# Kernel optimization log

Measured on AMD Instinct MI355X. Metric: run time of the kernel, lower is better.

Reference implementation:

```python
import jax, jax.numpy as jnp
import numpy as np

DIM = 256
HEADS = 8
DIM_HEAD = 64
SLICE_NUM = 64
INNER = HEADS * DIM_HEAD
B, N = 4, 32768


def setup_inputs() -> dict:
    key = jax.random.key(0)
    ks = jax.random.split(key, 12)
    s_in = 1.0 / np.sqrt(DIM)
    s_h = 1.0 / np.sqrt(DIM_HEAD)
    s_o = 1.0 / np.sqrt(INNER)
    return {
        "x": jax.random.normal(ks[0], (B, N, DIM), dtype=jnp.float32),
        "Wfx": jax.random.normal(ks[1], (INNER, DIM), dtype=jnp.float32) * s_in,
        "bfx": jax.random.normal(ks[2], (INNER,), dtype=jnp.float32) * 0.01,
        "Wx": jax.random.normal(ks[3], (INNER, DIM), dtype=jnp.float32) * s_in,
        "bx": jax.random.normal(ks[4], (INNER,), dtype=jnp.float32) * 0.01,
        "Wslice": jax.random.normal(ks[5], (SLICE_NUM, DIM_HEAD), dtype=jnp.float32) * s_h,
        "bslice": jax.random.normal(ks[6], (SLICE_NUM,), dtype=jnp.float32) * 0.01,
        "temperature": jnp.ones((1, HEADS, 1, 1), dtype=jnp.float32) * 0.5,
        "Wq": jax.random.normal(ks[7], (DIM_HEAD, DIM_HEAD), dtype=jnp.float32) * s_h,
        "Wk": jax.random.normal(ks[8], (DIM_HEAD, DIM_HEAD), dtype=jnp.float32) * s_h,
        "Wv": jax.random.normal(ks[9], (DIM_HEAD, DIM_HEAD), dtype=jnp.float32) * s_h,
        "Wout": jax.random.normal(ks[10], (DIM, INNER), dtype=jnp.float32) * s_o,
        "bout": jax.random.normal(ks[11], (DIM,), dtype=jnp.float32) * 0.01,
    }


def reference(x, Wfx, bfx, Wx, bx, Wslice, bslice, temperature, Wq, Wk, Wv, Wout, bout):
    b, n, c = x.shape
    Ch = Wq.shape[0]
    H = Wfx.shape[0] // Ch
    # project and split heads: [B, H, N, Ch]
    fx_mid = (x @ Wfx.T + bfx).reshape(b, n, H, Ch).transpose(0, 2, 1, 3)
    x_mid = (x @ Wx.T + bx).reshape(b, n, H, Ch).transpose(0, 2, 1, 3)
    # soft slice assignment: [B, H, N, M]
    temp = jnp.clip(temperature, 0.1, 5.0)
    logits = (x_mid @ Wslice.T + bslice) / temp
    sw = jax.nn.softmax(logits, axis=-1)
    sw = sw / (sw.sum(axis=2, keepdims=True) + 1e-5)  # normalize over N per slice
    # slice tokens: [B, H, M, Ch]
    slice_token = jnp.einsum('bhnc,bhng->bhgc', fx_mid, sw)
    # attention over slices
    q = slice_token @ Wq.T
    k = slice_token @ Wk.T
    v = slice_token @ Wv.T
    scale = Ch ** (-0.5)
    attn = jax.nn.softmax(jnp.einsum('bhgc,bhmc->bhgm', q, k) * scale, axis=-1)
    out_tok = attn @ v  # [B, H, M, Ch]
    # deslice back to N points
    out_x = jnp.einsum('bhgc,bhng->bhnc', out_tok, sw)
    out_x = out_x.transpose(0, 2, 1, 3).reshape(b, n, H * Ch)
    return out_x @ Wout.T + bout
```

## Files before the change

### kernel.cpp

```cpp
#include <hip/hip_runtime.h>
#include <hip/hip_bf16.h>

typedef __attribute__((ext_vector_type(8))) short bf16x8;
typedef __attribute__((ext_vector_type(4))) float f32x4;

union U16 { int4 v; ushort u[8]; };

__device__ __forceinline__ float b2f(ushort u){ return __uint_as_float(((unsigned int)u)<<16); }
__device__ __forceinline__ ushort f2b(float f){ return __bfloat16_as_ushort(__float2bfloat16(f)); }
__device__ __forceinline__ f32x4 mfma16(bf16x8 a, bf16x8 b, f32x4 c){
  return __builtin_amdgcn_mfma_f32_16x16x32_bf16(a,b,c,0,0,0);
}

__global__ void k_prep(const float* __restrict__ Wfx, const float* __restrict__ bfx,
                       const float* __restrict__ Wx,  const float* __restrict__ bx,
                       const float* __restrict__ Wout, const float* __restrict__ Wsl,
                       ushort* __restrict__ Wcat, float* __restrict__ bcat,
                       ushort* __restrict__ Wo16, ushort* __restrict__ Wsl16){
  int i = blockIdx.x*256 + threadIdx.x;
  if (i < 131072) Wcat[i] = f2b(Wfx[i]);
  else if (i < 262144) Wcat[i] = f2b(Wx[i-131072]);
  if (i < 131072) Wo16[i] = f2b(Wout[i]);
  if (i < 4096) Wsl16[i] = f2b(Wsl[i]);
  if (i < 512) bcat[i] = bfx[i];
  else if (i < 1024) bcat[i] = bx[i-512];
}

__global__ void k_zero(float* __restrict__ p, int n){
  int i = blockIdx.x*256 + threadIdx.x;
  if (i < n) p[i] = 0.f;
}

__global__ void k_xcvt(const float* __restrict__ x, ushort* __restrict__ xb){
  const size_t i = ((size_t)blockIdx.x*256 + threadIdx.x)*8;
  float4 a = *(const float4*)&x[i];
  float4 b = *(const float4*)&x[i+4];
  U16 o;
  o.u[0]=f2b(a.x); o.u[1]=f2b(a.y); o.u[2]=f2b(a.z); o.u[3]=f2b(a.w);
  o.u[4]=f2b(b.x); o.u[5]=f2b(b.y); o.u[6]=f2b(b.z); o.u[7]=f2b(b.w);
  *(int4*)&xb[i] = o.v;
}

__global__ __launch_bounds__(256,3) void k_proj(
    const ushort* __restrict__ xb, const ushort* __restrict__ Wcat,
    const float* __restrict__ bcat, ushort* __restrict__ fx, ushort* __restrict__ xm){
  __shared__ ushort lA[64*264];
  const int t = threadIdx.x;
  const int w=t>>6, l=t&63, l16=l&15, q8=l>>4;
  const int j0 = blockIdx.y*256 + w*64;
  const int srow = t>>5, scol = (t&31)*8;
  const long tokbase = (long)blockIdx.x*256;
  int4 stg[8];
  for (int i=0;i<8;i++)
    stg[i] = *(const int4*)&xb[(size_t)(tokbase + i*8 + srow)*256 + scol];
  for (int i=0;i<8;i++)
    *(int4*)&lA[(i*8+srow)*264 + scol] = stg[i];
  __syncthreads();
  for (int tt=0; tt<4; tt++){
    const long tok0 = tokbase + tt*64;
    if (tt<3){
      const long nt = tok0 + 64;
      for (int i=0;i<8;i++)
        stg[i] = *(const int4*)&xb[(size_t)(nt + i*8 + srow)*256 + scol];
    }
    f32x4 acc[4][4] = {};
    #pragma unroll 2
    for (int ks=0; ks<8; ks++){
      bf16x8 af[4], bfg[4];
      for (int i=0;i<4;i++) af[i] = *(const bf16x8*)&lA[(i*16+l16)*264 + ks*32 + q8*8];
      for (int j=0;j<4;j++) bfg[j] = *(const bf16x8*)&Wcat[(size_t)(j0+j*16+l16)*256 + ks*32 + q8*8];
      for (int i=0;i<4;i++)
        for (int j=0;j<4;j++)
          acc[i][j] = mfma16(af[i], bfg[j], acc[i][j]);
    }
    for (int j=0;j<4;j++){
      const int col = j0 + j*16 + l16;
      const float bc = bcat[col];
      ushort* dst = (col<512) ? fx : xm;
      const int cc = (col<512) ? col : col-512;
      for (int i=0;i<4;i++)
        for (int r=0;r<4;r++)
          dst[(size_t)(tok0 + i*16 + q8*4 + r)*512 + cc] = f2b(acc[i][j][r] + bc);
    }
    if (tt<3){
      __syncthreads();
      for (int i=0;i<8;i++)
        *(int4*)&lA[(i*8+srow)*264 + scol] = stg[i];
      __syncthreads();
    }
  }
}

__global__ __launch_bounds__(256,4) void k_slice(
    const ushort* __restrict__ xm, const ushort* __restrict__ Wsl16,
    const float* __restrict__ bslv, const float* __restrict__ temp,
    ushort* __restrict__ swn, float* __restrict__ cs){
  __shared__ float lcs[512];
  const int t = threadIdx.x, w=t>>6, l=t&63, l16=l&15, q8=l>>4;
  const long tok0 = (long)blockIdx.x*64;
  const int b = (int)(tok0 >> 15);
  for (int i=t;i<512;i+=256) lcs[i]=0.f;
  bf16x8 bw[4][2];
  for (int j=0;j<4;j++)
    for (int ks=0;ks<2;ks++)
      bw[j][ks] = *(const bf16x8*)&Wsl16[(j*16+l16)*64 + ks*32 + q8*8];
  float bj[4];
  for (int j=0;j<4;j++) bj[j] = bslv[j*16+l16];
  float itemp[8];
  for (int h=0;h<8;h++){
    float tp = temp[h]; tp = fminf(fmaxf(tp,0.1f),5.0f); itemp[h] = 1.0f/tp;
  }
  __syncthreads();
  const size_t rowbase = (size_t)(tok0 + w*16 + l16)*512;
  for (int h=0;h<8;h++){
    bf16x8 af0 = *(const bf16x8*)&xm[rowbase + h*64 + q8*8];
    bf16x8 af1 = *(const bf16x8*)&xm[rowbase + h*64 + 32 + q8*8];
    f32x4 acc[4] = {};
    for (int j=0;j<4;j++) acc[j] = mfma16(af0, bw[j][0], acc[j]);
    for (int j=0;j<4;j++) acc[j] = mfma16(af1, bw[j][1], acc[j]);
    const float it = itemp[h];
    float csum[4] = {0.f,0.f,0.f,0.f};
    for (int r=0;r<4;r++){
      float v[4]; float m = -1e30f;
      for (int j=0;j<4;j++){ v[j] = (acc[j][r] + bj[j])*it; m = fmaxf(m, v[j]); }
      for (int mk=1;mk<16;mk<<=1) m = fmaxf(m, __shfl_xor(m, mk, 64));
      float s = 0.f;
      for (int j=0;j<4;j++){ v[j] = __expf(v[j]-m); s += v[j]; }
      for (int mk=1;mk<16;mk<<=1) s += __shfl_xor(s, mk, 64);
      const float inv = 1.0f/s;
      const long tok = tok0 + w*16 + q8*4 + r;
      ushort* dst = &swn[((size_t)tok*8 + h)*64];
      for (int j=0;j<4;j++){
        float q = b2f(f2b(v[j]*inv));
        csum[j] += q;
        dst[j*16+l16] = f2b(q);
      }
    }
    for (int j=0;j<4;j++){
      float v = csum[j];
      v += __shfl_xor(v, 16, 64);
      v += __shfl_xor(v, 32, 64);
      if (q8==0) atomicAdd(&lcs[h*64 + j*16 + l16], v);
    }
  }
  __syncthreads();
  for (int i=t;i<512;i+=256) atomicAdd(&cs[(size_t)b*512 + i], lcs[i]);
}

__global__ __launch_bounds__(256,2) void k_accum(
    const ushort* __restrict__ swn, const ushort* __restrict__ fx,
    float* __restrict__ sraw){
  __shared__ ushort lW[64*136];
  __shared__ ushort lF[64*136];
  const int t = threadIdx.x;
  const int bh = blockIdx.y, b = bh>>3, h = bh&7;
  const long tokb = (long)b*32768 + (long)blockIdx.x*1024;
  const int w=t>>6, l=t&63, l16=l&15, q8=l>>4;
  const int nr = t>>3, g8 = (t&7)*8;
  f32x4 acc[4] = {};
  for (int sub=0; sub<8; sub++){
    __syncthreads();
    for (int ri=0; ri<4; ri++){
      const int nl = ri*32 + nr;
      const long tok = tokb + sub*128 + nl;
      U16 sv; sv.v = *(const int4*)&swn[((size_t)tok*8 + h)*64 + g8];
      U16 fv; fv.v = *(const int4*)&fx[(size_t)tok*512 + h*64 + g8];
      for (int j=0;j<8;j++){
        lW[(g8+j)*136 + nl] = sv.u[j];
        lF[(g8+j)*136 + nl] = fv.u[j];
      }
    }
    __syncthreads();
    #pragma unroll
    for (int kk=0; kk<4; kk++){
      bf16x8 af = *(const bf16x8*)&lW[(w*16+l16)*136 + kk*32 + q8*8];
      for (int j=0;j<4;j++){
        bf16x8 bfg = *(const bf16x8*)&lF[(j*16+l16)*136 + kk*32 + q8*8];
        acc[j] = mfma16(af, bfg, acc[j]);
      }
    }
  }
  for (int j=0;j<4;j++)
    for (int r=0;r<4;r++)
      atomicAdd(&sraw[((size_t)bh*64 + w*16 + q8*4 + r)*64 + j*16 + l16], acc[j][r]);
}

__global__ __launch_bounds__(256,1) void k_attn(
    const float* __restrict__ sraw, const float* __restrict__ cs,
    const float* __restrict__ Wq, const float* __restrict__ Wk, const float* __restrict__ Wv,
    ushort* __restrict__ ott){
  __shared__ float st[64*68], t1[64*68], t2[64*68];
  __shared__ ushort tw[64*68];
  __shared__ float pmax[256], psum[256], csl[64];
  const int t = threadIdx.x, bh = blockIdx.x;
  if (t < 64) csl[t] = 1.0f/(cs[bh*64+t] + 1e-5f);
  __syncthreads();
  for (int i=0;i<16;i++){ int idx=i*256+t; st[(idx>>6)*68+(idx&63)] = sraw[(size_t)bh*4096+idx]*csl[idx>>6]; }
  for (int i=0;i<16;i++){ int idx=i*256+t; tw[(idx>>6)*68+(idx&63)] = f2b(Wq[idx]); }
  __syncthreads();
  const int w=t>>6, lane=t&63;
  float o[16];
  #define GT(OUT) do{ for(int j=0;j<16;j++) OUT[j]=0.f; \
    for(int c4=0;c4<16;c4++){ float4 xv=*(float4*)&st[lane*68+c4*4]; \
      for(int j=0;j<16;j++){ ushort4 wv=*(const ushort4*)&tw[(w*16+j)*68+c4*4]; \
        OUT[j]+=xv.x*b2f(wv.x)+xv.y*b2f(wv.y)+xv.z*b2f(wv.z)+xv.w*b2f(wv.w);} } }while(0)
  GT(o);
  __syncthreads();
  for (int j=0;j<16;j++) t1[lane*68 + w*16+j] = o[j];
  for (int i=0;i<16;i++){ int idx=i*256+t; tw[(idx>>6)*68+(idx&63)] = f2b(Wk[idx]); }
  __syncthreads();
  GT(o);
  __syncthreads();
  for (int j=0;j<16;j++) t2[lane*68 + w*16+j] = o[j];
  __syncthreads();
  float sc[16];
  for (int j=0;j<16;j++) sc[j]=0.f;
  for (int c4=0;c4<16;c4++){
    float4 qv = *(float4*)&t1[lane*68+c4*4];
    for (int j=0;j<16;j++){
      float4 kv = *(float4*)&t2[(w*16+j)*68+c4*4];
      sc[j] += qv.x*kv.x + qv.y*kv.y + qv.z*kv.z + qv.w*kv.w;
    }
  }
  float pm = -1e30f;
  for (int j=0;j<16;j++){ sc[j]*=0.125f; pm=fmaxf(pm,sc[j]); }
  pmax[lane*4+w]=pm; __syncthreads();
  const float m = fmaxf(fmaxf(pmax[lane*4+0],pmax[lane*4+1]),fmaxf(pmax[lane*4+2],pmax[lane*4+3]));
  float s=0.f;
  for (int j=0;j<16;j++){ sc[j]=__expf(sc[j]-m); s+=sc[j]; }
  psum[lane*4+w]=s; __syncthreads();
  const float inv = 1.0f/(psum[lane*4+0]+psum[lane*4+1]+psum[lane*4+2]+psum[lane*4+3]);
  for (int j=0;j<16;j++) t1[lane*68 + w*16+j] = sc[j]*inv;
  for (int i=0;i<16;i++){ int idx=i*256+t; tw[(idx>>6)*68+(idx&63)] = f2b(Wv[idx]); }
  __syncthreads();
  GT(o);
  __syncthreads();
  for (int j=0;j<16;j++) t2[lane*68 + w*16+j] = o[j];
  __syncthreads();
  float ot[16];
  for (int j=0;j<16;j++) ot[j]=0.f;
  for (int m4=0;m4<16;m4++){
    float4 av = *(float4*)&t1[lane*68+m4*4];
    for (int j=0;j<16;j++){
      int c = w*16+j;
      ot[j] += av.x*t2[(m4*4+0)*68+c] + av.y*t2[(m4*4+1)*68+c]
             + av.z*t2[(m4*4+2)*68+c] + av.w*t2[(m4*4+3)*68+c];
    }
  }
  const float ics = csl[lane];
  for (int j=0;j<16;j++)
    ott[(size_t)bh*4096 + (size_t)(w*16+j)*64 + lane] = f2b(ot[j]*ics);
  #undef GT
}

__global__ __launch_bounds__(256,2) void k_deslice(
    const ushort* __restrict__ swn, const ushort* __restrict__ ott,
    ushort* __restrict__ ox){
  __shared__ ushort lS[32*520];
  const int t = threadIdx.x;
  const long tok0 = (long)blockIdx.x*32;
  const int b = (int)(tok0 >> 15);
  const int rw = t>>3, sg = t&7;
  for (int i=0;i<8;i++)
    *(int4*)&lS[rw*520 + i*64 + sg*8] = *(const int4*)&swn[(size_t)(tok0+rw)*512 + i*64 + sg*8];
  __syncthreads();
  const int w=t>>6, l=t&63, l16=l&15, q8=l>>4;
  for (int h=0; h<8; h++){
    const int bh = b*8 + h;
    f32x4 acc[2] = {};
    for (int kb=0; kb<2; kb++){
      bf16x8 bfg = *(const bf16x8*)&ott[(size_t)(bh*64 + w*16 + l16)*64 + kb*32 + q8*8];
      for (int i=0;i<2;i++){
        bf16x8 af = *(const bf16x8*)&lS[(i*16+l16)*520 + h*64 + kb*32 + q8*8];
        acc[i] = mfma16(af, bfg, acc[i]);
      }
    }
    for (int i=0;i<2;i++)
      for (int r=0;r<4;r++)
        ox[(size_t)(tok0 + i*16 + q8*4 + r)*512 + h*64 + w*16 + l16] = f2b(acc[i][r]);
  }
}

__global__ __launch_bounds__(256,2) void k_out(
    const ushort* __restrict__ ox, const ushort* __restrict__ Wo16,
    const float* __restrict__ bout, float* __restrict__ out){
  __shared__ ushort lA[32*520];
  const int t = threadIdx.x;
  const long tok0 = (long)blockIdx.x*32;
  const int rw = t>>3, sg = t&7;
  for (int i=0;i<8;i++)
    *(int4*)&lA[rw*520 + i*64 + sg*8] = *(const int4*)&ox[(size_t)(tok0+rw)*512 + i*64 + sg*8];
  __syncthreads();
  const int w=t>>6, l=t&63, l16=l&15, q8=l>>4;
  const int j0 = w*64;
  f32x4 acc[2][4] = {};
  #pragma unroll 2
  for (int ks=0; ks<16; ks++){
    bf16x8 af[2], bfg[4];
    for (int i=0;i<2;i++) af[i] = *(const bf16x8*)&lA[(i*16+l16)*520 + ks*32 + q8*8];
    for (int j=0;j<4;j++) bfg[j] = *(const bf16x8*)&Wo16[(size_t)(j0+j*16+l16)*512 + ks*32 + q8*8];
    for (int i=0;i<2;i++)
      for (int j=0;j<4;j++)
        acc[i][j] = mfma16(af[i], bfg[j], acc[i][j]);
  }
  for (int j=0;j<4;j++){
    const int col = j0 + j*16 + l16;
    const float bc = bout[col];
    for (int i=0;i<2;i++)
      for (int r=0;r<4;r++)
        out[(size_t)(tok0 + i*16 + q8*4 + r)*256 + col] = acc[i][j][r] + bc;
  }
}

extern "C" void kernel_launch(void* const* d_in, const int* in_sizes, int n_in,
                              void* d_out, int out_size, void* d_ws, size_t ws_size,
                              hipStream_t stream) {
  (void)in_sizes; (void)n_in; (void)out_size;
  const float* x    = (const float*)d_in[0];
  const float* Wfx  = (const float*)d_in[1];
  const float* bfx  = (const float*)d_in[2];
  const float* Wx   = (const float*)d_in[3];
  const float* bx   = (const float*)d_in[4];
  const float* Wsl  = (const float*)d_in[5];
  const float* bsl  = (const float*)d_in[6];
  const float* temp = (const float*)d_in[7];
  const float* Wq   = (const float*)d_in[8];
  const float* Wk   = (const float*)d_in[9];
  const float* Wv   = (const float*)d_in[10];
  const float* Wout = (const float*)d_in[11];
  const float* bout = (const float*)d_in[12];
  float* out = (float*)d_out;
  char* ws = (char*)d_ws;

  constexpr size_t O_FX   = 0;
  constexpr size_t O_XM   = 134217728;
  constexpr size_t O_SWN  = 268435456;
  constexpr size_t O_SRAW = 402653184;
  constexpr size_t O_CS   = O_SRAW + 524288;
  constexpr size_t O_OTT  = O_CS + 8192;
  constexpr size_t O_WCAT = O_OTT + 262144;
  constexpr size_t O_BCAT = O_WCAT + 524288;
  constexpr size_t O_WOUT = O_BCAT + 4096;
  constexpr size_t O_WSL  = O_WOUT + 262144;
  constexpr size_t NEED   = O_WSL + 8192;
  if (ws_size < NEED) return;

  ushort* fxb  = (ushort*)(ws + O_FX);
  ushort* xmb  = (ushort*)(ws + O_XM);
  ushort* swn  = (ushort*)(ws + O_SWN);
  ushort* xb   = (ushort*)(ws + O_SWN);
  float*  sraw = (float*)(ws + O_SRAW);
  float*  cs   = (float*)(ws + O_CS);
  ushort* ott  = (ushort*)(ws + O_OTT);
  ushort* Wcat = (ushort*)(ws + O_WCAT);
  float*  bcat = (float*)(ws + O_BCAT);
  ushort* Wo16 = (ushort*)(ws + O_WOUT);
  ushort* Wsl16= (ushort*)(ws + O_WSL);
  ushort* oxb  = xmb;

  k_prep<<<1024,256,0,stream>>>(Wfx,bfx,Wx,bx,Wout,Wsl,Wcat,bcat,Wo16,Wsl16);
  k_zero<<<520,256,0,stream>>>(sraw, 133120);
  k_xcvt<<<16384,256,0,stream>>>(x,xb);
  k_proj<<<dim3(512,4),256,0,stream>>>(xb,Wcat,bcat,fxb,xmb);
  k_slice<<<2048,256,0,stream>>>(xmb,Wsl16,bsl,temp,swn,cs);
  k_accum<<<dim3(32,32),256,0,stream>>>(swn,fxb,sraw);
  k_attn<<<32,256,0,stream>>>(sraw,cs,Wq,Wk,Wv,ott);
  k_deslice<<<4096,256,0,stream>>>(swn,ott,oxb);
  k_out<<<4096,256,0,stream>>>(oxb,Wo16,bout,out);
}
```

Baseline: 870.7 us.

## Retile projection and output GEMMs as 128x128 LDS double-buffered tiles

Both k_proj and k_out become conventional 128x128 output tiles over a 2x2 wave grid. A and B are staged through double-buffered LDS in 32-wide K slices, with the next slice prefetched into registers while the current one feeds MFMA. Previously weights were read straight from global memory per wave, and k_out only covered 32 tokens per block, so the goal is more operand reuse and less global and L2 traffic. k_deslice also hoists its per-head ott weight fragments into registers before the loop. This costs more registers, adds a barrier per K step, and the smaller K slices give less work per sync.

```diff
diff --git a/kernel.cpp b/kernel.cpp
--- a/kernel.cpp
+++ b/kernel.cpp
@@ -44,50 +44,53 @@
 __global__ __launch_bounds__(256,3) void k_proj(
     const ushort* __restrict__ xb, const ushort* __restrict__ Wcat,
     const float* __restrict__ bcat, ushort* __restrict__ fx, ushort* __restrict__ xm){
-  __shared__ ushort lA[64*264];
+  __shared__ ushort lA[2][128*40];
+  __shared__ ushort lB[2][128*40];
   const int t = threadIdx.x;
   const int w=t>>6, l=t&63, l16=l&15, q8=l>>4;
-  const int j0 = blockIdx.y*256 + w*64;
-  const int srow = t>>5, scol = (t&31)*8;
-  const long tokbase = (long)blockIdx.x*256;
-  int4 stg[8];
-  for (int i=0;i<8;i++)
-    stg[i] = *(const int4*)&xb[(size_t)(tokbase + i*8 + srow)*256 + scol];
-  for (int i=0;i<8;i++)
-    *(int4*)&lA[(i*8+srow)*264 + scol] = stg[i];
-  __syncthreads();
-  for (int tt=0; tt<4; tt++){
-    const long tok0 = tokbase + tt*64;
-    if (tt<3){
-      const long nt = tok0 + 64;
-      for (int i=0;i<8;i++)
-        stg[i] = *(const int4*)&xb[(size_t)(nt + i*8 + srow)*256 + scol];
-    }
-    f32x4 acc[4][4] = {};
-    #pragma unroll 2
-    for (int ks=0; ks<8; ks++){
-      bf16x8 af[4], bfg[4];
-      for (int i=0;i<4;i++) af[i] = *(const bf16x8*)&lA[(i*16+l16)*264 + ks*32 + q8*8];
-      for (int j=0;j<4;j++) bfg[j] = *(const bf16x8*)&Wcat[(size_t)(j0+j*16+l16)*256 + ks*32 + q8*8];
-      for (int i=0;i<4;i++)
-        for (int j=0;j<4;j++)
-          acc[i][j] = mfma16(af[i], bfg[j], acc[i][j]);
-    }
-    for (int j=0;j<4;j++){
-      const int col = j0 + j*16 + l16;
-      const float bc = bcat[col];
-      ushort* dst = (col<512) ? fx : xm;
-      const int cc = (col<512) ? col : col-512;
-      for (int i=0;i<4;i++)
-        for (int r=0;r<4;r++)
-          dst[(size_t)(tok0 + i*16 + q8*4 + r)*512 + cc] = f2b(acc[i][j][r] + bc);
-    }
-    if (tt<3){
-      __syncthreads();
-      for (int i=0;i<8;i++)
-        *(int4*)&lA[(i*8+srow)*264 + scol] = stg[i];
-      __syncthreads();
-    }
+  const int wm = w>>1, wn = w&1;
+  const long m0 = (long)blockIdx.x*128;
+  const int n0 = blockIdx.y*128;
+  const int srow = t>>2, sseg = (t&3)*8;
+  int4 a0,a1,b0,b1;
+  a0 = *(const int4*)&xb[(size_t)(m0+srow)*256 + sseg];
+  a1 = *(const int4*)&xb[(size_t)(m0+64+srow)*256 + sseg];
+  b0 = *(const int4*)&Wcat[(size_t)(n0+srow)*256 + sseg];
+  b1 = *(const int4*)&Wcat[(size_t)(n0+64+srow)*256 + sseg];
+  *(int4*)&lA[0][srow*40+sseg] = a0; *(int4*)&lA[0][(64+srow)*40+sseg] = a1;
+  *(int4*)&lB[0][srow*40+sseg] = b0; *(int4*)&lB[0][(64+srow)*40+sseg] = b1;
+  __syncthreads();
+  f32x4 acc[4][4] = {};
+  for (int ks=0; ks<8; ks++){
+    const int cur = ks&1, nxt = cur^1;
+    if (ks<7){
+      const int ko = (ks+1)*32;
+      a0 = *(const int4*)&xb[(size_t)(m0+srow)*256 + ko + sseg];
+      a1 = *(const int4*)&xb[(size_t)(m0+64+srow)*256 + ko + sseg];
+      b0 = *(const int4*)&Wcat[(size_t)(n0+srow)*256 + ko + sseg];
+      b1 = *(const int4*)&Wcat[(size_t)(n0+64+srow)*256 + ko + sseg];
+    }
+    bf16x8 af[4], bfg[4];
+    for (int i=0;i<4;i++) af[i]  = *(const bf16x8*)&lA[cur][(wm*64+i*16+l16)*40 + q8*8];
+    for (int j=0;j<4;j++) bfg[j] = *(const bf16x8*)&lB[cur][(wn*64+j*16+l16)*40 + q8*8];
+    for (int i=0;i<4;i++)
+      for (int j=0;j<4;j++)
+        acc[i][j] = mfma16(af[i], bfg[j], acc[i][j]);
+    if (ks<7){
+      *(int4*)&lA[nxt][srow*40+sseg] = a0; *(int4*)&lA[nxt][(64+srow)*40+sseg] = a1;
+      *(int4*)&lB[nxt][srow*40+sseg] = b0; *(int4*)&lB[nxt][(64+srow)*40+sseg] = b1;
+    }
+    __syncthreads();
+  }
+  ushort* dst = (n0 < 512) ? fx : xm;
+  const int nb = (n0 < 512) ? n0 : n0-512;
+  for (int j=0;j<4;j++){
+    const int colg = n0 + wn*64 + j*16 + l16;
+    const float bc = bcat[colg];
+    const int col = nb + wn*64 + j*16 + l16;
+    for (int i=0;i<4;i++)
+      for (int r=0;r<4;r++)
+        dst[(size_t)(m0 + wm*64 + i*16 + q8*4 + r)*512 + col] = f2b(acc[i][j][r] + bc);
   }
 }
 
@@ -260,19 +263,21 @@
   const int t = threadIdx.x;
   const long tok0 = (long)blockIdx.x*32;
   const int b = (int)(tok0 >> 15);
+  const int w=t>>6, l=t&63, l16=l&15, q8=l>>4;
+  bf16x8 bo[8][2];
+  for (int h=0;h<8;h++)
+    for (int kb=0;kb<2;kb++)
+      bo[h][kb] = *(const bf16x8*)&ott[(size_t)((b*8+h)*64 + w*16 + l16)*64 + kb*32 + q8*8];
   const int rw = t>>3, sg = t&7;
   for (int i=0;i<8;i++)
     *(int4*)&lS[rw*520 + i*64 + sg*8] = *(const int4*)&swn[(size_t)(tok0+rw)*512 + i*64 + sg*8];
   __syncthreads();
-  const int w=t>>6, l=t&63, l16=l&15, q8=l>>4;
   for (int h=0; h<8; h++){
-    const int bh = b*8 + h;
     f32x4 acc[2] = {};
     for (int kb=0; kb<2; kb++){
-      bf16x8 bfg = *(const bf16x8*)&ott[(size_t)(bh*64 + w*16 + l16)*64 + kb*32 + q8*8];
       for (int i=0;i<2;i++){
         bf16x8 af = *(const bf16x8*)&lS[(i*16+l16)*520 + h*64 + kb*32 + q8*8];
-        acc[i] = mfma16(af, bfg, acc[i]);
+        acc[i] = mfma16(af, bo[h][kb], acc[i]);
       }
     }
     for (int i=0;i<2;i++)
@@ -281,34 +286,59 @@
   }
 }
 
-__global__ __launch_bounds__(256,2) void k_out(
+__global__ __launch_bounds__(256,3) void k_out(
     const ushort* __restrict__ ox, const ushort* __restrict__ Wo16,
     const float* __restrict__ bout, float* __restrict__ out){
-  __shared__ ushort lA[32*520];
+  __shared__ ushort lA[2][128*40];
+  __shared__ ushort lB[2][128*40];
   const int t = threadIdx.x;
-  const long tok0 = (long)blockIdx.x*32;
-  const int rw = t>>3, sg = t&7;
-  for (int i=0;i<8;i++)
-    *(int4*)&lA[rw*520 + i*64 + sg*8] = *(const int4*)&ox[(size_t)(tok0+rw)*512 + i*64 + sg*8];
-  __syncthreads();
   const int w=t>>6, l=t&63, l16=l&15, q8=l>>4;
-  const int j0 = w*64;
+  const int wm = w>>1, wn = w&1;
+  const long m0 = (long)blockIdx.x*128;
+  const int n0 = blockIdx.y*128;
+  const int srow = t>>2, sseg = (t&3)*8;
+  int4 a0,a1,b0,b1;
+  a0 = *(const int4*)&ox[(size_t)(m0+srow)*512 + sseg];
+  a1 = *(const int4*)&ox[(size_t)(m0+64+srow)*512 + sseg];
+  b0 = *(const int4*)&Wo16[(size_t)(n0+srow)*512 + sseg];
+  b1 = *(const int4*)&Wo16[(size_t)(n0+64+srow)*512 + sseg];
+  *(int4*)&lA[0][srow*40+sseg] = a0; *(int4*)&lA[0][(64+srow)*40+sseg] = a1;
+  *(int4*)&lB[0][srow*40+sseg] = b0; *(int4*)&lB[0][(64+srow)*40+sseg] = b1;
+  __syncthreads();
   f32x4 acc[2][4] = {};
-  #pragma unroll 2
+  f32x4 acc2[2][4] = {};
   for (int ks=0; ks<16; ks++){
-    bf16x8 af[2], bfg[4];
-    for (int i=0;i<2;i++) af[i] = *(const bf16x8*)&lA[(i*16+l16)*520 + ks*32 + q8*8];
-    for (int j=0;j<4;j++) bfg[j] = *(const bf16x8*)&Wo16[(size_t)(j0+j*16+l16)*512 + ks*32 + q8*8];
-    for (int i=0;i<2;i++)
-      for (int j=0;j<4;j++)
-        acc[i][j] = mfma16(af[i], bfg[j], acc[i][j]);
+    const int cur = ks&1, nxt = cur^1;
+    if (ks<15){
+      const int ko = (ks+1)*32;
+      a0 = *(const int4*)&ox[(size_t)(m0+srow)*512 + ko + sseg];
+      a1 = *(const int4*)&ox[(size_t)(m0+64+srow)*512 + ko + sseg];
+      b0 = *(const int4*)&Wo16[(size_t)(n0+srow)*512 + ko + sseg];
+      b1 = *(const int4*)&Wo16[(size_t)(n0+64+srow)*512 + ko + sseg];
+    }
+    bf16x8 af[4], bfg[4];
+    for (int i=0;i<4;i++) af[i]  = *(const bf16x8*)&lA[cur][(wm*64+i*16+l16)*40 + q8*8];
+    for (int j=0;j<4;j++) bfg[j] = *(const bf16x8*)&lB[cur][(wn*64+j*16+l16)*40 + q8*8];
+    for (int j=0;j<4;j++){
+      acc[0][j]  = mfma16(af[0], bfg[j], acc[0][j]);
+      acc[1][j]  = mfma16(af[1], bfg[j], acc[1][j]);
+      acc2[0][j] = mfma16(af[2], bfg[j], acc2[0][j]);
+      acc2[1][j] = mfma16(af[3], bfg[j], acc2[1][j]);
+    }
+    if (ks<15){
+      *(int4*)&lA[nxt][srow*40+sseg] = a0; *(int4*)&lA[nxt][(64+srow)*40+sseg] = a1;
+      *(int4*)&lB[nxt][srow*40+sseg] = b0; *(int4*)&lB[nxt][(64+srow)*40+sseg] = b1;
+    }
+    __syncthreads();
   }
   for (int j=0;j<4;j++){
-    const int col = j0 + j*16 + l16;
+    const int col = n0 + wn*64 + j*16 + l16;
     const float bc = bout[col];
     for (int i=0;i<2;i++)
-      for (int r=0;r<4;r++)
-        out[(size_t)(tok0 + i*16 + q8*4 + r)*256 + col] = acc[i][j][r] + bc;
+      for (int r=0;r<4;r++){
+        out[(size_t)(m0 + wm*64 + i*16 + q8*4 + r)*256 + col] = acc[i][j][r] + bc;
+        out[(size_t)(m0 + wm*64 + (i+2)*16 + q8*4 + r)*256 + col] = acc2[i][j][r] + bc;
+      }
   }
 }
 
@@ -361,10 +391,10 @@
   k_prep<<<1024,256,0,stream>>>(Wfx,bfx,Wx,bx,Wout,Wsl,Wcat,bcat,Wo16,Wsl16);
   k_zero<<<520,256,0,stream>>>(sraw, 133120);
   k_xcvt<<<16384,256,0,stream>>>(x,xb);
-  k_proj<<<dim3(512,4),256,0,stream>>>(xb,Wcat,bcat,fxb,xmb);
+  k_proj<<<dim3(1024,8),256,0,stream>>>(xb,Wcat,bcat,fxb,xmb);
   k_slice<<<2048,256,0,stream>>>(xmb,Wsl16,bsl,temp,swn,cs);
   k_accum<<<dim3(32,32),256,0,stream>>>(swn,fxb,sraw);
   k_attn<<<32,256,0,stream>>>(sraw,cs,Wq,Wk,Wv,ott);
   k_deslice<<<4096,256,0,stream>>>(swn,ott,oxb);
-  k_out<<<4096,256,0,stream>>>(oxb,Wo16,bout,out);
-}
+  k_out<<<dim3(1024,2),256,0,stream>>>(oxb,Wo16,bout,out);
+}
```

Result: faster. 708.7 us (-18.6%).
